# Optimization experiments

Hardware: AMD Instinct MI355X
Metric: run time of the kernel (lower is better)

## Reference

```python
import jax, jax.numpy as jnp
import numpy as np

T, E, IN, OUT, A, R = 16384, 8, 1024, 1024, 8, 16  # tokens, experts, d_in, d_out, adapters, lora rank


def prepare_routing(x, indices, num_groups):
    """Sort tokens by group index; return sorted x, per-group counts, unsort map, sorted ids."""
    sort_idx = jnp.argsort(indices)  # stable sort keeps within-group order
    x_sorted = x[sort_idx]
    group_sizes = jnp.bincount(indices, length=num_groups).astype(jnp.int32)
    unsort_indices = jnp.argsort(sort_idx)
    return x_sorted, group_sizes, unsort_indices, indices[sort_idx]


def setup_inputs() -> dict:
    key = jax.random.key(0)
    ks = jax.random.split(key, 6)
    # tokens pre-sorted by expert: group_sizes must sum to T exactly
    expert_ids = jnp.sort(jax.random.randint(ks[0], (T,), 0, E))
    group_sizes = jnp.bincount(expert_ids, length=E).astype(jnp.int32)
    x = jax.random.normal(ks[1], (T, IN), jnp.float32)
    adapter_indices_sorted = jax.random.randint(ks[2], (T,), 0, A)
    weight = jax.random.normal(ks[3], (E, IN, OUT), jnp.float32) * 0.02
    lora_A = jax.random.normal(ks[4], (A, E, IN, R), jnp.float32) * 0.02
    lora_B = jax.random.normal(ks[5], (A, E, R, OUT), jnp.float32) * 0.02
    lora_scaling = jnp.ones((A,), jnp.float32)
    return {
        "x": x,
        "group_sizes": group_sizes,
        "adapter_indices_sorted": adapter_indices_sorted,
        "weight": weight,
        "lora_A": lora_A,
        "lora_B": lora_B,
        "lora_scaling": lora_scaling,
    }


def reference(x, group_sizes, adapter_indices_sorted, weight, lora_A, lora_B, lora_scaling):
    # base grouped GEMM over experts: [T,IN] x [E,IN,OUT] -> [T,OUT]
    base_out = jax.lax.ragged_dot(x, weight, group_sizes)

    # per-token expert id from contiguous group sizes
    expert_ids = jnp.repeat(jnp.arange(E), group_sizes, total_repeat_length=T)
    flattened = expert_ids * A + adapter_indices_sorted  # expert-major (E,A) group id

    # flatten adapters x experts into E*A groups (expert-major to match flattened ids)
    A_mat = lora_A.transpose(1, 0, 2, 3).reshape(E * A, IN, R)
    B_mat = lora_B.transpose(1, 0, 2, 3).reshape(E * A, R, OUT)

    x_sorted, combined_gs, unsort_indices, _ = prepare_routing(x, flattened, E * A)
    inter = jax.lax.ragged_dot(x_sorted, A_mat, combined_gs)          # [T,R]
    lora_out_sorted = jax.lax.ragged_dot(inter, B_mat, combined_gs)   # [T,OUT]
    lora_out = lora_out_sorted[unsort_indices]
    lora_out = lora_out * lora_scaling[adapter_indices_sorted][:, None]
    return base_out + lora_out
```

## Files before the change

kernel.cpp:

```cpp
#include <hip/hip_runtime.h>

#define T_TOK 16384
#define NEXP 8
#define DIN 1024
#define DOUT 1024
#define NADP 8
#define RANK 16
#define NGRP 64
#define MAXP1 520
#define BK 64
#define NKSTEP 16

typedef float f32x4 __attribute__((ext_vector_type(4)));
typedef float f32x16 __attribute__((ext_vector_type(16)));
typedef __bf16 bf16x8 __attribute__((ext_vector_type(8)));

typedef __attribute__((address_space(3))) void lds_void;
typedef __attribute__((address_space(1))) void g_void;

static __device__ __forceinline__ unsigned short f2bf(float f) {
    union { float f; unsigned u; } c; c.f = f;
    unsigned r = c.u + 0x7FFFu + ((c.u >> 16) & 1u);
    return (unsigned short)(r >> 16);
}

#define XB2 2048
#define NBW 2048
__global__ __launch_bounds__(256) void k_convert_all(const float* __restrict__ x,
                                                     const float* __restrict__ W,
                                                     const float* __restrict__ lA,
                                                     const float* __restrict__ lB,
                                                     unsigned short* __restrict__ xb,
                                                     unsigned short* __restrict__ Wt,
                                                     unsigned short* __restrict__ Agt,
                                                     unsigned short* __restrict__ Blt) {
    __shared__ __attribute__((aligned(16))) unsigned short lds_u[16 * 1032];
    int b = blockIdx.x;
    int t = threadIdx.x;
    if (b < XB2) {
        const size_t total = (size_t)(T_TOK + 128) * DIN / 4;
        const size_t conv  = (size_t)T_TOK * DIN / 4;
        size_t gid = (size_t)b * 256 + t;
#pragma unroll
        for (int it = 0; it < 9; it++) {
            size_t u = gid + (size_t)it * (XB2 * 256);
            if (u < total) {
                ushort4 o;
                if (u < conv) {
                    float4 v = *(const float4*)(x + u * 4);
                    o.x = f2bf(v.x); o.y = f2bf(v.y); o.z = f2bf(v.z); o.w = f2bf(v.w);
                } else {
                    o.x = 0; o.y = 0; o.z = 0; o.w = 0;
                }
                *(ushort4*)(xb + u * 4) = o;
            }
        }
    } else if (b < XB2 + NBW) {
        int idx = b - XB2;
        int e = idx >> 8;
        int k0 = ((idx >> 4) & 15) * 64, n0 = (idx & 15) * 64;
        const float* We = W + (size_t)e * DIN * DOUT;
        unsigned short* Wte = Wt + (size_t)e * DIN * DOUT;
        unsigned* lds32 = (unsigned*)lds_u;
        int kp = t >> 3;
        int nc = (t & 7) * 8;
        const float* r0 = We + (size_t)(k0 + 2 * kp) * DOUT + n0 + nc;
        const float* r1 = r0 + DOUT;
        float4 a0 = *(const float4*)r0, a1 = *(const float4*)(r0 + 4);
        float4 c0 = *(const float4*)r1, c1 = *(const float4*)(r1 + 4);
        lds32[(nc + 0) * 34 + kp] = (unsigned)f2bf(a0.x) | ((unsigned)f2bf(c0.x) << 16);
        lds32[(nc + 1) * 34 + kp] = (unsigned)f2bf(a0.y) | ((unsigned)f2bf(c0.y) << 16);
        lds32[(nc + 2) * 34 + kp] = (unsigned)f2bf(a0.z) | ((unsigned)f2bf(c0.z) << 16);
        lds32[(nc + 3) * 34 + kp] = (unsigned)f2bf(a0.w) | ((unsigned)f2bf(c0.w) << 16);
        lds32[(nc + 4) * 34 + kp] = (unsigned)f2bf(a1.x) | ((unsigned)f2bf(c1.x) << 16);
        lds32[(nc + 5) * 34 + kp] = (unsigned)f2bf(a1.y) | ((unsigned)f2bf(c1.y) << 16);
        lds32[(nc + 6) * 34 + kp] = (unsigned)f2bf(a1.z) | ((unsigned)f2bf(c1.z) << 16);
        lds32[(nc + 7) * 34 + kp] = (unsigned)f2bf(a1.w) | ((unsigned)f2bf(c1.w) << 16);
        __syncthreads();
        int n = t >> 2, kq = (t & 3) * 8;
        uint2 d0 = *(const uint2*)&lds32[n * 34 + kq + 0];
        uint2 d1 = *(const uint2*)&lds32[n * 34 + kq + 2];
        uint2 d2 = *(const uint2*)&lds32[n * 34 + kq + 4];
        uint2 d3 = *(const uint2*)&lds32[n * 34 + kq + 6];
        uint4 v0; v0.x = d0.x; v0.y = d0.y; v0.z = d1.x; v0.w = d1.y;
        uint4 v1; v1.x = d2.x; v1.y = d2.y; v1.z = d3.x; v1.w = d3.y;
        *(uint4*)(Wte + (size_t)(n0 + n) * DIN + k0 + kq * 2) = v0;
        *(uint4*)(Wte + (size_t)(n0 + n) * DIN + k0 + kq * 2 + 8) = v1;
    } else if (b < XB2 + NBW + NGRP) {
        int g = b - (XB2 + NBW);
        int a = g & 7, e = g >> 3;
        const float* src = lA + (size_t)(a * NEXP + e) * DIN * RANK;
#pragma unroll
        for (int it = 0; it < 4; it++) {
            int k = it * 256 + t;
            const float4* p = (const float4*)(src + (size_t)k * RANK);
            float4 v0 = p[0], v1 = p[1], v2 = p[2], v3 = p[3];
            lds_u[0 * 1032 + k] = f2bf(v0.x);  lds_u[1 * 1032 + k] = f2bf(v0.y);
            lds_u[2 * 1032 + k] = f2bf(v0.z);  lds_u[3 * 1032 + k] = f2bf(v0.w);
            lds_u[4 * 1032 + k] = f2bf(v1.x);  lds_u[5 * 1032 + k] = f2bf(v1.y);
            lds_u[6 * 1032 + k] = f2bf(v1.z);  lds_u[7 * 1032 + k] = f2bf(v1.w);
            lds_u[8 * 1032 + k] = f2bf(v2.x);  lds_u[9 * 1032 + k] = f2bf(v2.y);
            lds_u[10 * 1032 + k] = f2bf(v2.z); lds_u[11 * 1032 + k] = f2bf(v2.w);
            lds_u[12 * 1032 + k] = f2bf(v3.x); lds_u[13 * 1032 + k] = f2bf(v3.y);
            lds_u[14 * 1032 + k] = f2bf(v3.z); lds_u[15 * 1032 + k] = f2bf(v3.w);
        }
        __syncthreads();
        unsigned short* dst = Agt + (size_t)g * RANK * DIN;
        int r = t >> 4, ks = (t & 15) * 64;
#pragma unroll
        for (int j = 0; j < 8; j++)
            *(uint4*)(dst + r * DIN + ks + j * 8) = *(const uint4*)&lds_u[r * 1032 + ks + j * 8];
    } else {
        int idx = b - (XB2 + NBW + NGRP);
        int e = idx >> 3, nc = idx & 7;
        int k = t >> 1, half = t & 1;
        int a = k >> 4, r = k & 15;
        const float* src = lB + ((size_t)(a * NEXP + e) * RANK + r) * DOUT + nc * 128 + half * 64;
#pragma unroll
        for (int j = 0; j < 16; j++) {
            float4 v = *(const float4*)(src + j * 4);
            int nl = half * 64 + j * 4;
            lds_u[k * 129 + nl + 0] = f2bf(v.x);
            lds_u[k * 129 + nl + 1] = f2bf(v.y);
            lds_u[k * 129 + nl + 2] = f2bf(v.z);
            lds_u[k * 129 + nl + 3] = f2bf(v.w);
        }
        __syncthreads();
        int nl = t >> 1, kh = t & 1;
        unsigned short* dst = Blt + ((size_t)(e * 1024 + nc * 128 + nl)) * 128 + kh * 64;
#pragma unroll
        for (int g2 = 0; g2 < 8; g2++) {
            uint4 pv;
            unsigned short s0 = lds_u[(kh * 64 + g2 * 8 + 0) * 129 + nl];
            unsigned short s1 = lds_u[(kh * 64 + g2 * 8 + 1) * 129 + nl];
            unsigned short s2 = lds_u[(kh * 64 + g2 * 8 + 2) * 129 + nl];
            unsigned short s3 = lds_u[(kh * 64 + g2 * 8 + 3) * 129 + nl];
            unsigned short s4 = lds_u[(kh * 64 + g2 * 8 + 4) * 129 + nl];
            unsigned short s5 = lds_u[(kh * 64 + g2 * 8 + 5) * 129 + nl];
            unsigned short s6 = lds_u[(kh * 64 + g2 * 8 + 6) * 129 + nl];
            unsigned short s7 = lds_u[(kh * 64 + g2 * 8 + 7) * 129 + nl];
            pv.x = (unsigned)s0 | ((unsigned)s1 << 16);
            pv.y = (unsigned)s2 | ((unsigned)s3 << 16);
            pv.z = (unsigned)s4 | ((unsigned)s5 << 16);
            pv.w = (unsigned)s6 | ((unsigned)s7 << 16);
            *(uint4*)(dst + g2 * 8) = pv;
        }
    }
}

__global__ __launch_bounds__(256) void k_pass1(const unsigned short* __restrict__ xb,
                                               const unsigned short* __restrict__ Agt,
                                               const int* __restrict__ gs,
                                               const int* __restrict__ aidx,
                                               const float* __restrict__ scal,
                                               unsigned short* __restrict__ interb) {
    int bid = blockIdx.x;
    int e = -1, m0 = 0, valid = 0;
    {
        int acc_t = 0, base = 0;
#pragma unroll
        for (int ee = 0; ee < NEXP; ee++) {
            int sz = gs[ee];
            int nt = (sz + 31) >> 5;
            if (e < 0 && bid < acc_t + nt) {
                int loc = bid - acc_t;
                e = ee; m0 = base + (loc << 5);
                int v = sz - (loc << 5); valid = v > 32 ? 32 : v;
            }
            acc_t += nt; base += sz;
        }
    }
    if (e < 0) return;

    int t = threadIdx.x;
    int lane = t & 63, w = t >> 6;
    int ln = lane & 15, q = lane >> 4;

    const unsigned short* A0 = Agt + ((size_t)(e * NADP + 2 * w) * RANK + ln) * DIN + q * 8;
    const unsigned short* A1 = A0 + (size_t)RANK * DIN;
    const unsigned short* X0 = xb + (size_t)(m0 + ln) * DIN + q * 8;

    f32x4 acc[2][2];
#pragma unroll
    for (int i = 0; i < 2; i++) {
        acc[i][0] = (f32x4){0.f, 0.f, 0.f, 0.f};
        acc[i][1] = (f32x4){0.f, 0.f, 0.f, 0.f};
    }

#pragma unroll 4
    for (int k0 = 0; k0 < DIN; k0 += 32) {
        bf16x8 b0 = *(const bf16x8*)(A0 + k0);
        bf16x8 b1 = *(const bf16x8*)(A1 + k0);
#pragma unroll
        for (int rg = 0; rg < 2; rg++) {
            bf16x8 af = *(const bf16x8*)(X0 + (size_t)(rg * 16) * DIN + k0);
            acc[rg][0] = __builtin_amdgcn_mfma_f32_16x16x32_bf16(b0, af, acc[rg][0], 0, 0, 0);
            acc[rg][1] = __builtin_amdgcn_mfma_f32_16x16x32_bf16(b1, af, acc[rg][1], 0, 0, 0);
        }
    }

    float s0 = scal[2 * w], s1 = scal[2 * w + 1];
#pragma unroll
    for (int rg = 0; rg < 2; rg++) {
        int tr = rg * 16 + ln;
        if (tr < valid) {
            int tok = m0 + tr;
            int a = aidx[tok];
            if (a == 2 * w) {
                f32x4 v = acc[rg][0];
                ushort4 u;
                u.x = f2bf(s0 * v[0]); u.y = f2bf(s0 * v[1]);
                u.z = f2bf(s0 * v[2]); u.w = f2bf(s0 * v[3]);
                *(ushort4*)(interb + (size_t)tok * RANK + q * 4) = u;
            } else if (a == 2 * w + 1) {
                f32x4 v = acc[rg][1];
                ushort4 u;
                u.x = f2bf(s1 * v[0]); u.y = f2bf(s1 * v[1]);
                u.z = f2bf(s1 * v[2]); u.w = f2bf(s1 * v[3]);
                *(ushort4*)(interb + (size_t)tok * RANK + q * 4) = u;
            }
        }
    }
}

__global__ __launch_bounds__(256) void k_gemm(const unsigned short* __restrict__ xb,
                                              const unsigned short* __restrict__ wt,
                                              const int* __restrict__ gs,
                                              const unsigned short* __restrict__ interb,
                                              const int* __restrict__ aidx,
                                              const unsigned short* __restrict__ Blt,
                                              float* __restrict__ out) {
    __shared__ __attribute__((aligned(16))) unsigned short smem[32768];

    int id = blockIdx.y * 8 + blockIdx.x;
    int xcd = id & 7;
    int j = id >> 3;
    int tileid = xcd * 17 + (j >> 3);
    int n0 = (j & 7) * 128;

    int e = -1, m0 = 0, valid = 0;
    {
        int acc_t = 0, base = 0;
#pragma unroll
        for (int ee = 0; ee < NEXP; ee++) {
            int sz = gs[ee];
            int nt = (sz + 127) >> 7;
            if (e < 0 && tileid < acc_t + nt) {
                int loc = tileid - acc_t;
                e = ee; m0 = base + (loc << 7);
                int v = sz - (loc << 7); valid = v > 128 ? 128 : v;
            }
            acc_t += nt; base += sz;
        }
    }
    if (e < 0) return;

    int t = threadIdx.x;
    int lane = t & 63;
    int wave = t >> 6;
    int wm = wave >> 1, wn = wave & 1;
    int r32 = lane & 31, hi = lane >> 5;

    const unsigned short* wte = wt + (size_t)e * DIN * DOUT;

    f32x16 acc[2][2];
#pragma unroll
    for (int i = 0; i < 2; i++)
#pragma unroll
        for (int j2 = 0; j2 < 2; j2++) acc[i][j2] = (f32x16)(0.f);

    int srow[4], skoff[4];
#pragma unroll
    for (int j3 = 0; j3 < 4; j3++) {
        srow[j3]  = j3 * 32 + wave * 8 + (lane >> 3);
        skoff[j3] = ((lane & 7) ^ (srow[j3] & 7)) * 8;
    }

    auto STAGE = [&](int buf, int k0) {
#pragma unroll
        for (int j3 = 0; j3 < 4; j3++) {
            __builtin_amdgcn_global_load_lds(
                (const g_void*)(xb + (size_t)(m0 + srow[j3]) * DIN + k0 + skoff[j3]),
                (lds_void*)((char*)smem + buf * 32768 + j3 * 4096 + wave * 1024), 16, 0, 0);
            __builtin_amdgcn_global_load_lds(
                (const g_void*)(wte + (size_t)(n0 + srow[j3]) * DIN + k0 + skoff[j3]),
                (lds_void*)((char*)smem + buf * 32768 + 16384 + j3 * 4096 + wave * 1024), 16, 0, 0);
        }
    };

    auto COMPUTE = [&](int buf) {
        const char* Ab = (const char*)smem + buf * 32768;
        const char* Bb = Ab + 16384;
        __builtin_amdgcn_s_setprio(1);
#pragma unroll
        for (int kf = 0; kf < 4; kf++) {
            int kc = kf * 2 + hi;
            int slot = kc ^ (r32 & 7);
            bf16x8 af[2], bfr[2];
#pragma unroll
            for (int mi = 0; mi < 2; mi++) {
                int row = wm * 64 + mi * 32 + r32;
                af[mi] = *(const bf16x8*)(Ab + row * 128 + slot * 16);
            }
#pragma unroll
            for (int ni = 0; ni < 2; ni++) {
                int row = wn * 64 + ni * 32 + r32;
                bfr[ni] = *(const bf16x8*)(Bb + row * 128 + slot * 16);
            }
#pragma unroll
            for (int mi = 0; mi < 2; mi++)
#pragma unroll
                for (int ni = 0; ni < 2; ni++)
                    acc[mi][ni] = __builtin_amdgcn_mfma_f32_32x32x16_bf16(af[mi], bfr[ni], acc[mi][ni], 0, 0, 0);
        }
        __builtin_amdgcn_s_setprio(0);
    };

    STAGE(0, 0);
    STAGE(1, BK);
#pragma unroll
    for (int ts = 0; ts < NKSTEP; ts++) {
        if (ts < NKSTEP - 1) asm volatile("s_waitcnt vmcnt(8)" ::: "memory");
        else                 asm volatile("s_waitcnt vmcnt(0)" ::: "memory");
        __builtin_amdgcn_s_barrier();
        COMPUTE(ts & 1);
        if (ts < NKSTEP - 2) {
            __builtin_amdgcn_s_barrier();
            STAGE(ts & 1, (ts + 2) * BK);
        }
    }

    {
        int row = t >> 1, h = t & 1;
        int rs = row & 15;
        uint4 z = {0u, 0u, 0u, 0u};
        uint4 payload = z;
        int pslot = -1;
        if (row < valid) {
            int tok = m0 + row;
            int a = aidx[tok];
            payload = *(const uint4*)(interb + (size_t)tok * RANK + h * 8);
            pslot = a * 2 + h;
        }
#pragma unroll
        for (int l2 = 0; l2 < 8; l2++) {
            int l = l2 * 2 + h;
            int phys = l ^ rs;
            *(uint4*)((char*)smem + row * 256 + phys * 16) = (l == pslot) ? payload : z;
        }
    }
    __syncthreads();
#pragma unroll
    for (int kf = 0; kf < 8; kf++) {
        int kc = kf * 2 + hi;
        bf16x8 af[2], bfr[2];
#pragma unroll
        for (int ni = 0; ni < 2; ni++) {
            int n = wn * 64 + ni * 32 + r32;
            bfr[ni] = *(const bf16x8*)(Blt + ((size_t)(e * 1024 + n0 + n)) * 128 + kc * 8);
        }
#pragma unroll
        for (int mi = 0; mi < 2; mi++) {
            int row = wm * 64 + mi * 32 + r32;
            int slot = kc ^ (r32 & 15);
            af[mi] = *(const bf16x8*)((const char*)smem + row * 256 + slot * 16);
        }
#pragma unroll
        for (int mi = 0; mi < 2; mi++)
#pragma unroll
            for (int ni = 0; ni < 2; ni++)
                acc[mi][ni] = __builtin_amdgcn_mfma_f32_32x32x16_bf16(af[mi], bfr[ni], acc[mi][ni], 0, 0, 0);
    }

#pragma unroll
    for (int mi = 0; mi < 2; mi++) {
#pragma unroll
        for (int r = 0; r < 16; r++) {
            int row32 = (r & 3) + 8 * (r >> 2) + 4 * hi;
            int row_l = wm * 64 + mi * 32 + row32;
            if (row_l < valid) {
                float* orow = out + (size_t)(m0 + row_l) * DOUT + n0 + wn * 64 + r32;
#pragma unroll
                for (int ni = 0; ni < 2; ni++)
                    orow[ni * 32] = acc[mi][ni][r];
            }
        }
    }
}

extern "C" void kernel_launch(void* const* d_in, const int* in_sizes, int n_in,
                              void* d_out, int out_size, void* d_ws, size_t ws_size,
                              hipStream_t stream) {
    (void)in_sizes; (void)n_in; (void)out_size; (void)ws_size;
    const float* x    = (const float*)d_in[0];
    const int*   gs   = (const int*)d_in[1];
    const int*   aidx = (const int*)d_in[2];
    const float* W    = (const float*)d_in[3];
    const float* lA   = (const float*)d_in[4];
    const float* lB   = (const float*)d_in[5];
    const float* scal = (const float*)d_in[6];
    float* out = (float*)d_out;

    char* ws = (char*)d_ws;
    unsigned short* xb     = (unsigned short*)ws;        size_t o = 33816576;
    unsigned short* wt     = (unsigned short*)(ws + o);  o += 16777216;
    unsigned short* Agt    = (unsigned short*)(ws + o);  o += 2097152;
    unsigned short* Blt    = (unsigned short*)(ws + o);  o += 2097152;
    unsigned short* interb = (unsigned short*)(ws + o);  o += 524288;

    k_convert_all<<<XB2 + NBW + NGRP + 64, 256, 0, stream>>>(x, W, lA, lB, xb, wt, Agt, Blt);
    k_pass1<<<MAXP1, 256, 0, stream>>>(xb, Agt, gs, aidx, scal, interb);
    k_gemm<<<dim3(8, 136), 256, 0, stream>>>(xb, wt, gs, interb, aidx, Blt, out);
}
```

Before: 264.9 us.

## Halve K tile and use four-buffer LDS ring with three-stage prefetch

The base GEMM K tile drops from 64 to 32, so there are twice as many K steps. Shared memory becomes a ring of four 16KB buffers, with three stages of global-to-LDS loads in flight instead of two. The XOR swizzle for the staging addresses and the fragment reads is rebuilt to fit the narrower 64-byte rows. The aim is to hide more global-load latency at the same total LDS size. The cost is twice as many barriers and wait points per K pass, with less MFMA work between each one.

```diff
diff --git a/kernel.cpp b/kernel.cpp
--- a/kernel.cpp
+++ b/kernel.cpp
@@ -8,8 +8,8 @@
 #define RANK 16
 #define NGRP 64
 #define MAXP1 520
-#define BK 64
-#define NKSTEP 16
+#define BK 32
+#define NKSTEP 32
 
 typedef float f32x4 __attribute__((ext_vector_type(4)));
 typedef float f32x16 __attribute__((ext_vector_type(16)));
@@ -269,43 +269,44 @@
 #pragma unroll
         for (int j2 = 0; j2 < 2; j2++) acc[i][j2] = (f32x16)(0.f);
 
-    int srow[4], skoff[4];
-#pragma unroll
-    for (int j3 = 0; j3 < 4; j3++) {
-        srow[j3]  = j3 * 32 + wave * 8 + (lane >> 3);
-        skoff[j3] = ((lane & 7) ^ (srow[j3] & 7)) * 8;
-    }
+    int srow = wave * 16 + (lane >> 2);
+    int skoff = (((lane & 3) ^ ((lane >> 2) ^ (lane >> 4)) ) & 3) * 8;
+    const unsigned short* gA = xb + (size_t)m0 * DIN;
+    const unsigned short* gB = wte + (size_t)n0 * DIN;
 
     auto STAGE = [&](int buf, int k0) {
 #pragma unroll
-        for (int j3 = 0; j3 < 4; j3++) {
+        for (int jj = 0; jj < 2; jj++) {
+            int row = jj * 64 + srow;
             __builtin_amdgcn_global_load_lds(
-                (const g_void*)(xb + (size_t)(m0 + srow[j3]) * DIN + k0 + skoff[j3]),
-                (lds_void*)((char*)smem + buf * 32768 + j3 * 4096 + wave * 1024), 16, 0, 0);
+                (const g_void*)(gA + (size_t)row * DIN + k0 + skoff),
+                (lds_void*)((char*)smem + buf * 16384 + jj * 4096 + wave * 1024), 16, 0, 0);
             __builtin_amdgcn_global_load_lds(
-                (const g_void*)(wte + (size_t)(n0 + srow[j3]) * DIN + k0 + skoff[j3]),
-                (lds_void*)((char*)smem + buf * 32768 + 16384 + j3 * 4096 + wave * 1024), 16, 0, 0);
+                (const g_void*)(gB + (size_t)row * DIN + k0 + skoff),
+                (lds_void*)((char*)smem + buf * 16384 + 8192 + jj * 4096 + wave * 1024), 16, 0, 0);
         }
     };
 
+    int fr = (r32 ^ (r32 >> 2)) & 3;
+
     auto COMPUTE = [&](int buf) {
-        const char* Ab = (const char*)smem + buf * 32768;
-        const char* Bb = Ab + 16384;
+        const char* Ab = (const char*)smem + buf * 16384;
+        const char* Bb = Ab + 8192;
         __builtin_amdgcn_s_setprio(1);
 #pragma unroll
-        for (int kf = 0; kf < 4; kf++) {
+        for (int kf = 0; kf < 2; kf++) {
             int kc = kf * 2 + hi;
-            int slot = kc ^ (r32 & 7);
+            int slot = (kc ^ fr) * 16;
             bf16x8 af[2], bfr[2];
 #pragma unroll
             for (int mi = 0; mi < 2; mi++) {
                 int row = wm * 64 + mi * 32 + r32;
-                af[mi] = *(const bf16x8*)(Ab + row * 128 + slot * 16);
+                af[mi] = *(const bf16x8*)(Ab + row * 64 + slot);
             }
 #pragma unroll
             for (int ni = 0; ni < 2; ni++) {
                 int row = wn * 64 + ni * 32 + r32;
-                bfr[ni] = *(const bf16x8*)(Bb + row * 128 + slot * 16);
+                bfr[ni] = *(const bf16x8*)(Bb + row * 64 + slot);
             }
 #pragma unroll
             for (int mi = 0; mi < 2; mi++)
@@ -317,16 +318,18 @@
     };
 
     STAGE(0, 0);
-    STAGE(1, BK);
+    STAGE(1, 32);
+    STAGE(2, 64);
 #pragma unroll
     for (int ts = 0; ts < NKSTEP; ts++) {
-        if (ts < NKSTEP - 1) asm volatile("s_waitcnt vmcnt(8)" ::: "memory");
-        else                 asm volatile("s_waitcnt vmcnt(0)" ::: "memory");
+        if (ts < NKSTEP - 2)      asm volatile("s_waitcnt vmcnt(8)" ::: "memory");
+        else if (ts == NKSTEP - 2) asm volatile("s_waitcnt vmcnt(4)" ::: "memory");
+        else                       asm volatile("s_waitcnt vmcnt(0)" ::: "memory");
         __builtin_amdgcn_s_barrier();
-        COMPUTE(ts & 1);
-        if (ts < NKSTEP - 2) {
+        COMPUTE(ts & 3);
+        if (ts < NKSTEP - 3) {
             __builtin_amdgcn_s_barrier();
-            STAGE(ts & 1, (ts + 2) * BK);
+            STAGE((ts + 3) & 3, (ts + 3) * BK);
         }
     }
 
```

New measurement: 269.3 us. About the same (+1.7%).
